# Performance work log

Measured on AMD Instinct MI355X. Metric: run time of the kernel, lower is better.

Reference implementation:

```python
import jax, jax.numpy as jnp
import numpy as np

B_, S, D = 2, 2048, 2048
F_ = 8192
R = 16
H = 16
HD = D // H
MOD_SCALE = 0.1
EPS = 1e-6


def _rmsnorm(x, w):
    v = jnp.mean(x * x, axis=-1, keepdims=True)
    return x * jax.lax.rsqrt(v + EPS) * w


def setup_inputs() -> dict:
    key = jax.random.key(0)
    ks = jax.random.split(key, 12)
    sd = 0.02
    return {
        "hidden_states": jax.random.normal(ks[0], (B_, S, D), jnp.float32),
        "ln1_w": jnp.ones((D,), jnp.float32),
        "ln2_w": jnp.ones((D,), jnp.float32),
        "Wq": jax.random.normal(ks[1], (D, D), jnp.float32) * sd,
        "Wk": jax.random.normal(ks[2], (D, D), jnp.float32) * sd,
        "Wv": jax.random.normal(ks[3], (D, D), jnp.float32) * sd,
        "Wo": jax.random.normal(ks[4], (D, D), jnp.float32) * sd,
        "A": jax.random.normal(ks[5], (D, R), jnp.float32) * (0.01 / np.sqrt(D)),
        "B": jax.random.normal(ks[6], (R, F_), jnp.float32) * (0.01 / np.sqrt(R)),
        "W_in_base": jax.random.normal(ks[7], (F_, D), jnp.float32) * sd,
        "W_up_base": jax.random.normal(ks[8], (F_, D), jnp.float32) * sd,
        "W_down": jax.random.normal(ks[9], (D, F_), jnp.float32) * sd,
    }


def _attention(x, Wq, Wk, Wv, Wo):
    # x: (b, s, d). Causal multi-head self-attention, torch Linear convention (y = x @ W.T).
    b, s, d = x.shape
    q = (x @ Wq.T).reshape(b, s, H, HD)
    k = (x @ Wk.T).reshape(b, s, H, HD)
    v = (x @ Wv.T).reshape(b, s, H, HD)
    scores = jnp.einsum("bqhd,bkhd->bhqk", q, k) / np.sqrt(HD).astype(np.float32)
    causal = jnp.tril(jnp.ones((s, s), bool))
    scores = jnp.where(causal, scores, jnp.finfo(scores.dtype).min)
    probs = jax.nn.softmax(scores, axis=-1)
    out = jnp.einsum("bhqk,bkhd->bqhd", probs, v).reshape(b, s, d)
    return out @ Wo.T


def reference(hidden_states, ln1_w, ln2_w, Wq, Wk, Wv, Wo, A, B, W_in_base, W_up_base, W_down):
    residual = hidden_states
    x = _rmsnorm(hidden_states, ln1_w)
    attn = _attention(x, Wq, Wk, Wv, Wo)  # (b, s, d)

    # NeuroPlasticComponent: delta_w[b,s,d,f] = sum_r mod[b,s,r] * A[d,r] * B[r,f]
    mod = MOD_SCALE * jnp.tanh(attn @ A)  # (b, s, r)

    # NPT quirk: post_attention_layernorm is applied to the ORIGINAL residual,
    # and attention output is never added into the residual stream.
    h = _rmsnorm(residual, ln2_w)  # (b, s, d)

    # Per-token modulated gate: (W_in_base + delta_w[b,s].T) @ h
    # delta_w[b,s].T @ h = sum_d delta[d,f] h[d] = ((mod * (h @ A)) @ B)[f]
    gate_pre = h @ W_in_base.T + (mod * (h @ A)) @ B  # (b, s, f)
    gate = jax.nn.silu(gate_pre)
    up = h @ W_up_base.T
    mlp_out = (gate * up) @ W_down.T
    return residual + mlp_out
```

## Files before the change

kernel.cpp:

```cpp
#include <hip/hip_runtime.h>

#define DI __device__ __forceinline__

typedef short s16x8 __attribute__((ext_vector_type(8)));
typedef float f32x4 __attribute__((ext_vector_type(4)));

typedef __attribute__((address_space(1))) const unsigned int as1_cuint;
typedef __attribute__((address_space(3))) unsigned int as3_uint;

DI unsigned short f2bf(float f) {
  union { float f; unsigned int u; } v; v.f = f;
  unsigned int r = v.u + 0x7fffu + ((v.u >> 16) & 1u);
  return (unsigned short)(r >> 16);
}
DI float bf2f(unsigned short b) {
  union { unsigned int u; float f; } v; v.u = ((unsigned int)b) << 16;
  return v.f;
}

DI void gl_lds16(const void* g, void* l) {
  __builtin_amdgcn_global_load_lds((as1_cuint*)g, (as3_uint*)l, 16, 0, 0);
}

DI void bar() {
  __builtin_amdgcn_sched_barrier(0);
  __builtin_amdgcn_s_barrier();
  __builtin_amdgcn_sched_barrier(0);
}
DI void vm0() { asm volatile("s_waitcnt vmcnt(0)" ::: "memory"); }
DI void vm2() { asm volatile("s_waitcnt vmcnt(2)" ::: "memory"); }
DI void vm4() { asm volatile("s_waitcnt vmcnt(4)" ::: "memory"); }
DI void vm6() { asm volatile("s_waitcnt vmcnt(6)" ::: "memory"); }

#define MFMA __builtin_amdgcn_mfma_f32_16x16x32_bf16

__global__ __launch_bounds__(256) void cvt_f32_bf16(const float* __restrict__ src,
                                                    unsigned short* __restrict__ dst, int n4) {
  int i = blockIdx.x * blockDim.x + threadIdx.x;
  int stride = gridDim.x * blockDim.x;
  for (; i < n4; i += stride) {
    float4 v = ((const float4*)src)[i];
    ((ushort4*)dst)[i] = make_ushort4(f2bf(v.x), f2bf(v.y), f2bf(v.z), f2bf(v.w));
  }
}

__global__ __launch_bounds__(256) void rmsnorm_dual(const float* __restrict__ hs,
                                                    const float* __restrict__ w1,
                                                    const float* __restrict__ w2,
                                                    unsigned short* __restrict__ xo,
                                                    unsigned short* __restrict__ ho) {
  const int D = 2048;
  int t = blockIdx.x, tid = threadIdx.x;
  const float* row = hs + (size_t)t * D;
  float4 a = ((const float4*)row)[tid * 2];
  float4 b = ((const float4*)row)[tid * 2 + 1];
  float ss = a.x * a.x + a.y * a.y + a.z * a.z + a.w * a.w +
             b.x * b.x + b.y * b.y + b.z * b.z + b.w * b.w;
#pragma unroll
  for (int off = 32; off; off >>= 1) ss += __shfl_xor(ss, off);
  __shared__ float red[4];
  int wave = tid >> 6, lane = tid & 63;
  if (lane == 0) red[wave] = ss;
  __syncthreads();
  float tot = red[0] + red[1] + red[2] + red[3];
  float inv = rsqrtf(tot / (float)D + 1e-6f);
  int base = tid * 8;
  float vals[8] = {a.x, a.y, a.z, a.w, b.x, b.y, b.z, b.w};
  float4 w1a = ((const float4*)(w1 + base))[0];
  float4 w1b = ((const float4*)(w1 + base))[1];
  float4 w2a = ((const float4*)(w2 + base))[0];
  float4 w2b = ((const float4*)(w2 + base))[1];
  float w1v[8] = {w1a.x, w1a.y, w1a.z, w1a.w, w1b.x, w1b.y, w1b.z, w1b.w};
  float w2v[8] = {w2a.x, w2a.y, w2a.z, w2a.w, w2b.x, w2b.y, w2b.z, w2b.w};
  unsigned short ox[8], oh[8];
#pragma unroll
  for (int j = 0; j < 8; ++j) {
    float n = vals[j] * inv;
    ox[j] = f2bf(n * w1v[j]);
    oh[j] = f2bf(n * w2v[j]);
  }
  ushort4* xp = (ushort4*)(xo + (size_t)t * D + base);
  ushort4* hp = (ushort4*)(ho + (size_t)t * D + base);
  xp[0] = make_ushort4(ox[0], ox[1], ox[2], ox[3]);
  xp[1] = make_ushort4(ox[4], ox[5], ox[6], ox[7]);
  hp[0] = make_ushort4(oh[0], oh[1], oh[2], oh[3]);
  hp[1] = make_ushort4(oh[4], oh[5], oh[6], oh[7]);
}

#define E_NONE 0
#define E_RES 3

template <int EPI>
__global__ __launch_bounds__(512, 2) void gemm_n128(
    const unsigned short* __restrict__ Amat, const unsigned short* __restrict__ Bt,
    int N, int K, int NT,
    unsigned short* __restrict__ Cbf, float* __restrict__ Cf,
    const float* __restrict__ Res) {
  __shared__ __align__(16) unsigned short lds[49152];
  int tid = threadIdx.x, lane = tid & 63;
  int w = tid >> 6, wm = w >> 2, wn = w & 3;
  int lr = lane & 15, g = lane >> 4;
  int nbn = N >> 7, nwg = gridDim.x, wg = blockIdx.x;
  int cpx = nwg >> 3;
  int swz = (wg & 7) * cpx + (wg >> 3);
  int tm = swz / nbn, tn = swz - tm * nbn;
  size_t m0 = (size_t)tm * 256, n0 = (size_t)tn * 128;

  int boffA[4][2], boffB[2][2];
#pragma unroll
  for (int mi = 0; mi < 4; ++mi)
#pragma unroll
    for (int kh = 0; kh < 2; ++kh) {
      int row = mi * 32 + wm * 16 + lr;
      boffA[mi][kh] = row * 128 + ((kh * 64 + g * 16) ^ ((row & 7) << 4));
    }
#pragma unroll
  for (int ni = 0; ni < 2; ++ni)
#pragma unroll
    for (int kh = 0; kh < 2; ++kh) {
      int row = ni * 64 + wn * 16 + lr;
      boffB[ni][kh] = row * 128 + ((kh * 64 + g * 16) ^ ((row & 7) << 4));
    }
  const char* ldsb = (const char*)lds;

  int srow = tid >> 3;
  int scb = ((tid & 7) * 16) ^ ((srow & 7) << 4);
  const unsigned short* pA0 = Amat + (m0 + srow) * (size_t)K + (scb >> 1);
  const unsigned short* pA1 = pA0 + (size_t)128 * K;
  const unsigned short* pB  = Bt + (n0 + srow) * (size_t)K + (scb >> 1);
  const size_t jst = (size_t)64 * K;
  int dst = w * 512;

  f32x4 acc[8][2] = {};

  auto stg = [&](const unsigned short* p, int BUF, int SLOT) {
    gl_lds16(p, &lds[BUF * 24576 + SLOT * 8192 + dst]);
    gl_lds16(p + jst, &lds[BUF * 24576 + SLOT * 8192 + 4096 + dst]);
  };

  stg(pA0, 0, 0); stg(pB, 0, 2); stg(pA1, 0, 1);
  pA0 += 64; pA1 += 64; pB += 64;
  vm2();
  bar();

  auto tile = [&](int t, int BUF) {
    s16x8 afr[4][2], bfr[2][2];
#pragma unroll
    for (int mi = 0; mi < 4; ++mi)
#pragma unroll
      for (int kh = 0; kh < 2; ++kh)
        afr[mi][kh] = *(const s16x8*)(ldsb + BUF * 49152 + 0 * 16384 + boffA[mi][kh]);
#pragma unroll
    for (int ni = 0; ni < 2; ++ni)
#pragma unroll
      for (int kh = 0; kh < 2; ++kh)
        bfr[ni][kh] = *(const s16x8*)(ldsb + BUF * 49152 + 2 * 16384 + boffB[ni][kh]);
    if (t + 1 < NT) { stg(pA0, BUF ^ 1, 0); stg(pB, BUF ^ 1, 2); }
    bar();
    __builtin_amdgcn_s_setprio(1);
#pragma unroll
    for (int mi = 0; mi < 4; ++mi)
#pragma unroll
      for (int ni = 0; ni < 2; ++ni)
#pragma unroll
        for (int kh = 0; kh < 2; ++kh)
          acc[mi][ni] = MFMA(afr[mi][kh], bfr[ni][kh], acc[mi][ni], 0, 0, 0);
    __builtin_amdgcn_s_setprio(0);
    if (t + 1 < NT) vm4(); else vm0();
    bar();
#pragma unroll
    for (int mi = 0; mi < 4; ++mi)
#pragma unroll
      for (int kh = 0; kh < 2; ++kh)
        afr[mi][kh] = *(const s16x8*)(ldsb + BUF * 49152 + 1 * 16384 + boffA[mi][kh]);
    if (t + 1 < NT) stg(pA1, BUF ^ 1, 1);
    bar();
    __builtin_amdgcn_s_setprio(1);
#pragma unroll
    for (int mi = 0; mi < 4; ++mi)
#pragma unroll
      for (int ni = 0; ni < 2; ++ni)
#pragma unroll
        for (int kh = 0; kh < 2; ++kh)
          acc[4 + mi][ni] = MFMA(afr[mi][kh], bfr[ni][kh], acc[4 + mi][ni], 0, 0, 0);
    __builtin_amdgcn_s_setprio(0);
    if (t + 1 < NT) vm2();
    bar();
    pA0 += 64; pA1 += 64; pB += 64;
  };

  for (int t = 0; t < NT; t += 2) { tile(t, 0); tile(t + 1, 1); }

#pragma unroll
  for (int mh = 0; mh < 2; ++mh)
#pragma unroll
    for (int mi = 0; mi < 4; ++mi)
#pragma unroll
      for (int r = 0; r < 4; ++r) {
        size_t row = m0 + mh * 128 + mi * 32 + wm * 16 + g * 4 + r;
#pragma unroll
        for (int ni = 0; ni < 2; ++ni) {
          size_t col = n0 + ni * 64 + wn * 16 + lr;
          float v = acc[mh * 4 + mi][ni][r];
          if constexpr (EPI == E_RES) Cf[row * N + col] = Res[row * N + col] + v;
          else Cbf[row * N + col] = f2bf(v);
        }
      }
}

__global__ __launch_bounds__(512, 2) void gemm_mlp256(
    const unsigned short* __restrict__ Hm, const unsigned short* __restrict__ Wg,
    const unsigned short* __restrict__ Wu,
    const float* __restrict__ cvec, const float* __restrict__ Bsm,
    unsigned short* __restrict__ Out) {
  const int N = 8192, K = 2048, NT = 32;
  __shared__ __align__(16) unsigned short lds[65536];
  int tid = threadIdx.x, lane = tid & 63;
  int w = tid >> 6, wm = w >> 2, wn = w & 3;
  int lr = lane & 15, g = lane >> 4;
  int nbn = N >> 7, nwg = gridDim.x, wg = blockIdx.x;
  int cpx = nwg >> 3;
  int swz = (wg & 7) * cpx + (wg >> 3);
  int tm = swz / nbn, tn = swz - tm * nbn;
  size_t m0 = (size_t)tm * 256, n0 = (size_t)tn * 128;

  int boffA[4][2], boffB[2][2];
#pragma unroll
  for (int mi = 0; mi < 4; ++mi)
#pragma unroll
    for (int kh = 0; kh < 2; ++kh) {
      int row = mi * 32 + wm * 16 + lr;
      boffA[mi][kh] = row * 128 + ((kh * 64 + g * 16) ^ ((row & 7) << 4));
    }
#pragma unroll
  for (int ni = 0; ni < 2; ++ni)
#pragma unroll
    for (int kh = 0; kh < 2; ++kh) {
      int row = ni * 64 + wn * 16 + lr;
      boffB[ni][kh] = row * 128 + ((kh * 64 + g * 16) ^ ((row & 7) << 4));
    }
  const char* ldsb = (const char*)lds;

  int srow = tid >> 3;
  int scb = ((tid & 7) * 16) ^ ((srow & 7) << 4);
  const unsigned short* pA0 = Hm + (m0 + srow) * (size_t)K + (scb >> 1);
  const unsigned short* pA1 = pA0 + (size_t)128 * K;
  const unsigned short* pBg = Wg + (n0 + srow) * (size_t)K + (scb >> 1);
  const unsigned short* pBu = Wu + (n0 + srow) * (size_t)K + (scb >> 1);
  const size_t jst = (size_t)64 * K;
  int dst = w * 512;

  f32x4 ag[8][2] = {}, au[8][2] = {};

  auto stg = [&](const unsigned short* p, int BUF, int SLOT) {
    gl_lds16(p, &lds[BUF * 32768 + SLOT * 8192 + dst]);
    gl_lds16(p + jst, &lds[BUF * 32768 + SLOT * 8192 + 4096 + dst]);
  };

  stg(pA0, 0, 0); stg(pBg, 0, 2); stg(pBu, 0, 3); stg(pA1, 0, 1);
  pA0 += 64; pA1 += 64; pBg += 64; pBu += 64;
  vm4();
  bar();

  auto tile = [&](int t, int BUF) {
    s16x8 afr[4][2], bg[2][2], bu[2][2];
#pragma unroll
    for (int mi = 0; mi < 4; ++mi)
#pragma unroll
      for (int kh = 0; kh < 2; ++kh)
        afr[mi][kh] = *(const s16x8*)(ldsb + BUF * 65536 + 0 * 16384 + boffA[mi][kh]);
#pragma unroll
    for (int ni = 0; ni < 2; ++ni)
#pragma unroll
      for (int kh = 0; kh < 2; ++kh)
        bg[ni][kh] = *(const s16x8*)(ldsb + BUF * 65536 + 2 * 16384 + boffB[ni][kh]);
    if (t + 1 < NT) { stg(pA0, BUF ^ 1, 0); stg(pBg, BUF ^ 1, 2); }
    bar();
    __builtin_amdgcn_s_setprio(1);
#pragma unroll
    for (int mi = 0; mi < 4; ++mi)
#pragma unroll
      for (int ni = 0; ni < 2; ++ni)
#pragma unroll
        for (int kh = 0; kh < 2; ++kh)
          ag[mi][ni] = MFMA(afr[mi][kh], bg[ni][kh], ag[mi][ni], 0, 0, 0);
    __builtin_amdgcn_s_setprio(0);
    if (t + 1 < NT) vm6(); else vm2();
    bar();
#pragma unroll
    for (int ni = 0; ni < 2; ++ni)
#pragma unroll
      for (int kh = 0; kh < 2; ++kh)
        bu[ni][kh] = *(const s16x8*)(ldsb + BUF * 65536 + 3 * 16384 + boffB[ni][kh]);
    if (t + 1 < NT) stg(pBu, BUF ^ 1, 3);
    bar();
    __builtin_amdgcn_s_setprio(1);
#pragma unroll
    for (int mi = 0; mi < 4; ++mi)
#pragma unroll
      for (int ni = 0; ni < 2; ++ni)
#pragma unroll
        for (int kh = 0; kh < 2; ++kh)
          au[mi][ni] = MFMA(afr[mi][kh], bu[ni][kh], au[mi][ni], 0, 0, 0);
    __builtin_amdgcn_s_setprio(0);
    if (t + 1 < NT) vm6(); else vm0();
    bar();
#pragma unroll
    for (int mi = 0; mi < 4; ++mi)
#pragma unroll
      for (int kh = 0; kh < 2; ++kh)
        afr[mi][kh] = *(const s16x8*)(ldsb + BUF * 65536 + 1 * 16384 + boffA[mi][kh]);
    if (t + 1 < NT) stg(pA1, BUF ^ 1, 1);
    bar();
    __builtin_amdgcn_s_setprio(1);
#pragma unroll
    for (int mi = 0; mi < 4; ++mi)
#pragma unroll
      for (int ni = 0; ni < 2; ++ni)
#pragma unroll
        for (int kh = 0; kh < 2; ++kh)
          ag[4 + mi][ni] = MFMA(afr[mi][kh], bg[ni][kh], ag[4 + mi][ni], 0, 0, 0);
    __builtin_amdgcn_s_setprio(0);
    bar();
    __builtin_amdgcn_s_setprio(1);
#pragma unroll
    for (int mi = 0; mi < 4; ++mi)
#pragma unroll
      for (int ni = 0; ni < 2; ++ni)
#pragma unroll
        for (int kh = 0; kh < 2; ++kh)
          au[4 + mi][ni] = MFMA(afr[mi][kh], bu[ni][kh], au[4 + mi][ni], 0, 0, 0);
    __builtin_amdgcn_s_setprio(0);
    if (t + 1 < NT) vm4();
    bar();
    pA0 += 64; pA1 += 64; pBg += 64; pBu += 64;
  };

  for (int t = 0; t < NT; t += 2) { tile(t, 0); tile(t + 1, 1); }

  float* cl = (float*)lds;
  float* bl = (float*)&lds[32768];
#pragma unroll
  for (int j = 0; j < 2; ++j) {
    int fi = tid * 2 + j;
    ((float4*)cl)[fi] = ((const float4*)(cvec + m0 * 16))[fi];
  }
  {
    int fi = tid;
    ((float4*)bl)[fi] = *(const float4*)(Bsm + (size_t)(fi >> 5) * N + n0 + (fi & 31) * 4);
  }
  bar();

#pragma unroll
  for (int mh = 0; mh < 2; ++mh)
#pragma unroll
    for (int mi = 0; mi < 4; ++mi)
#pragma unroll
      for (int r = 0; r < 4; ++r) {
        int rr = mh * 128 + mi * 32 + wm * 16 + g * 4 + r;
        size_t row = m0 + rr;
#pragma unroll
        for (int ni = 0; ni < 2; ++ni) {
          int cc = ni * 64 + wn * 16 + lr;
          size_t col = n0 + cc;
          float s = 0.f;
#pragma unroll
          for (int jj = 0; jj < 16; ++jj) s += cl[rr * 16 + jj] * bl[jj * 128 + cc];
          float gg = ag[mh * 4 + mi][ni][r] + s;
          float sig = 1.f / (1.f + __expf(-gg));
          Out[row * N + col] = f2bf(gg * sig * au[mh * 4 + mi][ni][r]);
        }
      }
}

__global__ __launch_bounds__(256) void vtrans(const unsigned short* __restrict__ qkv,
                                              unsigned short* __restrict__ vT) {
  __shared__ unsigned short t[64][72];
  int bh = blockIdx.z, b = bh >> 4, h = bh & 15;
  int k0 = blockIdx.x * 64, d0 = blockIdx.y * 64;
  int tid = threadIdx.x;
#pragma unroll
  for (int j = 0; j < 2; ++j) {
    int idx = tid + j * 256;
    int r = idx >> 3, c8 = (idx & 7) * 8;
    s16x8 v = *(const s16x8*)(qkv + ((size_t)(b * 2048 + k0 + r)) * 6144 + 4096 + h * 128 + d0 + c8);
#pragma unroll
    for (int e = 0; e < 8; ++e) t[r][c8 + e] = (unsigned short)v[e];
  }
  __syncthreads();
#pragma unroll
  for (int j = 0; j < 2; ++j) {
    int idx = tid + j * 256;
    int dr = idx >> 3, k8 = (idx & 7) * 8;
    s16x8 o;
#pragma unroll
    for (int e = 0; e < 8; ++e) o[e] = (short)t[k8 + e][dr];
    *(s16x8*)(vT + (size_t)bh * 262144 + (size_t)(d0 + dr) * 2048 + k0 + k8) = o;
  }
}

__global__ __launch_bounds__(256, 2) void attn_fwd2(const unsigned short* __restrict__ qkv,
                                                    const unsigned short* __restrict__ vT,
                                                    unsigned short* __restrict__ attn) {
  const int LD = 6144;
  __shared__ __align__(16) unsigned short Kt[8192];
  __shared__ __align__(16) unsigned short Vt[8192];
  __shared__ __align__(16) unsigned short Pl[4096];
  int tid = threadIdx.x, w = tid >> 6, lane = tid & 63;
  int lrow = lane & 15, g = lane >> 4;
  int qp = blockIdx.x, bh = blockIdx.y, b = bh >> 4, h = bh & 15;
  const unsigned short* Qb = qkv + (size_t)b * 2048 * LD + h * 128;
  const unsigned short* Kb = Qb + 2048;
  const unsigned short* vTb = vT + (size_t)bh * 262144;
  const float scale = 0.08838834764831845f;

#pragma unroll
  for (int pass = 0; pass < 2; ++pass) {
    int qtile = pass ? (31 - qp) : qp;
    int wq0 = qtile * 64 + w * 16;
    s16x8 qf[4];
#pragma unroll
    for (int kc = 0; kc < 4; ++kc)
      qf[kc] = *(const s16x8*)(Qb + (size_t)(wq0 + lrow) * LD + kc * 32 + g * 8);
    f32x4 ao[8] = {};
    float m_r[4], l_r[4];
#pragma unroll
    for (int r = 0; r < 4; ++r) { m_r[r] = -1e30f; l_r[r] = 0.f; }
    int nkt = qtile + 1;

    for (int kt = 0; kt < nkt; ++kt) {
      int k0 = kt * 64;
      bar();
#pragma unroll
      for (int j = 0; j < 4; ++j) {
        int o = j * 4096 + tid * 16;
        int row = o >> 8, cb = o & 255;
        int scb = cb ^ ((row & 7) << 4);
        gl_lds16(Kb + (size_t)(k0 + row) * LD + (scb >> 1), &Kt[(j * 4096 + w * 1024) >> 1]);
      }
#pragma unroll
      for (int j = 0; j < 4; ++j) {
        int o = j * 4096 + tid * 16;
        int row = o >> 7, cb = o & 127;
        int scb = cb ^ ((row & 7) << 4);
        gl_lds16(vTb + (size_t)row * 2048 + k0 + (scb >> 1), &Vt[(j * 4096 + w * 1024) >> 1]);
      }
      vm0();
      bar();
      f32x4 sa[4] = {};
#pragma unroll
      for (int ni = 0; ni < 4; ++ni)
#pragma unroll
        for (int kc = 0; kc < 4; ++kc) {
          int row = ni * 16 + lrow;
          int cb = kc * 64 + g * 16;
          int scb = cb ^ ((row & 7) << 4);
          s16x8 kf = *(const s16x8*)&Kt[row * 128 + (scb >> 1)];
          sa[ni] = MFMA(qf[kc], kf, sa[ni], 0, 0, 0);
        }
      if (k0 + 63 > wq0) {
#pragma unroll
        for (int ni = 0; ni < 4; ++ni)
#pragma unroll
          for (int r = 0; r < 4; ++r) {
            int q_idx = wq0 + g * 4 + r, k_idx = k0 + ni * 16 + lrow;
            float sv = sa[ni][r] * scale;
            sa[ni][r] = (k_idx > q_idx) ? -1e30f : sv;
          }
      } else {
#pragma unroll
        for (int ni = 0; ni < 4; ++ni)
#pragma unroll
          for (int r = 0; r < 4; ++r) sa[ni][r] *= scale;
      }
      float mt[4];
#pragma unroll
      for (int r = 0; r < 4; ++r)
        mt[r] = fmaxf(fmaxf(sa[0][r], sa[1][r]), fmaxf(sa[2][r], sa[3][r]));
#pragma unroll
      for (int r = 0; r < 4; ++r)
#pragma unroll
        for (int off = 8; off; off >>= 1) mt[r] = fmaxf(mt[r], __shfl_xor(mt[r], off));
      float al[4];
#pragma unroll
      for (int r = 0; r < 4; ++r) {
        float mn = fmaxf(m_r[r], mt[r]);
        al[r] = __expf(m_r[r] - mn);
        m_r[r] = mn;
      }
      float rs[4] = {0.f, 0.f, 0.f, 0.f};
#pragma unroll
      for (int ni = 0; ni < 4; ++ni)
#pragma unroll
        for (int r = 0; r < 4; ++r) {
          float p = __expf(sa[ni][r] - m_r[r]);
          rs[r] += p;
          int q = g * 4 + r, k = ni * 16 + lrow;
          Pl[w * 1024 + q * 64 + (k ^ ((q & 7) << 3))] = f2bf(p);
        }
#pragma unroll
      for (int r = 0; r < 4; ++r) {
#pragma unroll
        for (int off = 8; off; off >>= 1) rs[r] += __shfl_xor(rs[r], off);
        l_r[r] = l_r[r] * al[r] + rs[r];
      }
#pragma unroll
      for (int df = 0; df < 8; ++df)
#pragma unroll
        for (int r = 0; r < 4; ++r) ao[df][r] *= al[r];
      asm volatile("s_waitcnt lgkmcnt(0)" ::: "memory");
      __builtin_amdgcn_sched_barrier(0);
      s16x8 pa[2];
#pragma unroll
      for (int ks = 0; ks < 2; ++ks)
        pa[ks] = *(const s16x8*)&Pl[w * 1024 + lrow * 64 + ((ks * 32 + g * 8) ^ ((lrow & 7) << 3))];
#pragma unroll
      for (int df = 0; df < 8; ++df) {
#pragma unroll
        for (int ks = 0; ks < 2; ++ks) {
          int row = df * 16 + lrow;
          int cb = ks * 64 + g * 16;
          int scb = cb ^ ((row & 7) << 4);
          s16x8 vf = *(const s16x8*)&Vt[row * 64 + (scb >> 1)];
          ao[df] = MFMA(pa[ks], vf, ao[df], 0, 0, 0);
        }
      }
    }
#pragma unroll
    for (int df = 0; df < 8; ++df)
#pragma unroll
      for (int r = 0; r < 4; ++r) {
        int q = wq0 + g * 4 + r;
        float v = ao[df][r] / l_r[r];
        attn[((size_t)b * 2048 + q) * 2048 + h * 128 + df * 16 + lrow] = f2bf(v);
      }
    bar();
  }
}

__global__ __launch_bounds__(256) void modc(const unsigned short* __restrict__ attnO,
                                            const unsigned short* __restrict__ h,
                                            const float* __restrict__ A,
                                            float* __restrict__ cvec) {
  const int D = 2048;
  int t = blockIdx.x * 4 + (threadIdx.x >> 6);
  int lane = threadIdx.x & 63;
  float aA[16] = {}, aH[16] = {};
  for (int i = 0; i < D / 64; ++i) {
    int d = i * 64 + lane;
    float av = bf2f(attnO[(size_t)t * D + d]);
    float hv = bf2f(h[(size_t)t * D + d]);
    const float* ar = A + (size_t)d * 16;
#pragma unroll
    for (int j = 0; j < 16; ++j) {
      float a = ar[j];
      aA[j] += av * a;
      aH[j] += hv * a;
    }
  }
#pragma unroll
  for (int j = 0; j < 16; ++j) {
#pragma unroll
    for (int off = 32; off; off >>= 1) {
      aA[j] += __shfl_xor(aA[j], off);
      aH[j] += __shfl_xor(aH[j], off);
    }
  }
#pragma unroll
  for (int j = 0; j < 16; ++j)
    if (lane == j) cvec[(size_t)t * 16 + j] = 0.1f * tanhf(aA[j]) * aH[j];
}

extern "C" void kernel_launch(void* const* d_in, const int* in_sizes, int n_in,
                              void* d_out, int out_size, void* d_ws, size_t ws_size,
                              hipStream_t stream) {
  const float* hs  = (const float*)d_in[0];
  const float* ln1 = (const float*)d_in[1];
  const float* ln2 = (const float*)d_in[2];
  const float* Wq  = (const float*)d_in[3];
  const float* Wk  = (const float*)d_in[4];
  const float* Wv  = (const float*)d_in[5];
  const float* Wo  = (const float*)d_in[6];
  const float* Am  = (const float*)d_in[7];
  const float* Bm  = (const float*)d_in[8];
  const float* Win = (const float*)d_in[9];
  const float* Wup = (const float*)d_in[10];
  const float* Wdn = (const float*)d_in[11];
  float* out = (float*)d_out;
  (void)in_sizes; (void)n_in;

  const int T = 4096;
  const int Dm = 2048, F = 8192;
  const size_t MB = (size_t)1 << 20;

  const size_t need = 184 * MB;
  if (ws_size < need) {
    hipMemsetAsync(d_out, 0, (size_t)out_size * 4, stream);
    return;
  }
  char* base = (char*)d_ws;
  unsigned short* tb    = (unsigned short*)(base);
  unsigned short* wqkv  = (unsigned short*)(base);
  unsigned short* vT    = (unsigned short*)(base);
  unsigned short* xb    = (unsigned short*)(base + 24 * MB);
  unsigned short* attnO = (unsigned short*)(base + 40 * MB);
  unsigned short* qkv   = (unsigned short*)(base + 64 * MB);
  unsigned short* win   = (unsigned short*)(base + 64 * MB);
  unsigned short* wo    = (unsigned short*)(base + 112 * MB);
  unsigned short* hb    = (unsigned short*)(base + 120 * MB);
  unsigned short* attn  = (unsigned short*)(base + 136 * MB);
  float*          cv    = (float*)(base + 136 * MB);
  unsigned short* wup   = (unsigned short*)(base + 152 * MB);
  unsigned short* wdn   = (unsigned short*)(base + 152 * MB);

  cvt_f32_bf16<<<2048, 256, 0, stream>>>(Wq, wqkv, Dm * Dm / 4);
  cvt_f32_bf16<<<2048, 256, 0, stream>>>(Wk, wqkv + (size_t)Dm * Dm, Dm * Dm / 4);
  cvt_f32_bf16<<<2048, 256, 0, stream>>>(Wv, wqkv + (size_t)2 * Dm * Dm, Dm * Dm / 4);
  cvt_f32_bf16<<<2048, 256, 0, stream>>>(Wo, wo, Dm * Dm / 4);
  rmsnorm_dual<<<T, 256, 0, stream>>>(hs, ln1, ln2, xb, hb);

  gemm_n128<E_NONE><<<(T / 256) * (3 * Dm / 128), 512, 0, stream>>>(
      xb, wqkv, 3 * Dm, Dm, Dm / 64, qkv, nullptr, nullptr);

  vtrans<<<dim3(32, 2, 32), 256, 0, stream>>>(qkv, vT);
  attn_fwd2<<<dim3(16, 32), 256, 0, stream>>>(qkv, vT, attn);

  gemm_n128<E_NONE><<<(T / 256) * (Dm / 128), 512, 0, stream>>>(
      attn, wo, Dm, Dm, Dm / 64, attnO, nullptr, nullptr);

  modc<<<T / 4, 256, 0, stream>>>(attnO, hb, Am, cv);

  cvt_f32_bf16<<<2048, 256, 0, stream>>>(Win, win, F * Dm / 4);
  cvt_f32_bf16<<<2048, 256, 0, stream>>>(Wup, wup, F * Dm / 4);

  gemm_mlp256<<<(T / 256) * (F / 128), 512, 0, stream>>>(hb, win, wup, cv, Bm, tb);

  cvt_f32_bf16<<<2048, 256, 0, stream>>>(Wdn, wdn, Dm * F / 4);
  gemm_n128<E_RES><<<(T / 256) * (Dm / 128), 512, 0, stream>>>(
      tb, wdn, Dm, F, F / 64, nullptr, out, hs);
}
```

Before: 792.0 us.

## Issue all next-tile prefetches at once and merge gate/up MFMA phases

```diff
diff --git a/kernel.cpp b/kernel.cpp
--- a/kernel.cpp
+++ b/kernel.cpp
@@ -29,8 +29,8 @@
 }
 DI void vm0() { asm volatile("s_waitcnt vmcnt(0)" ::: "memory"); }
 DI void vm2() { asm volatile("s_waitcnt vmcnt(2)" ::: "memory"); }
-DI void vm4() { asm volatile("s_waitcnt vmcnt(4)" ::: "memory"); }
 DI void vm6() { asm volatile("s_waitcnt vmcnt(6)" ::: "memory"); }
+DI void vm8() { asm volatile("s_waitcnt vmcnt(8)" ::: "memory"); }
 
 #define MFMA __builtin_amdgcn_mfma_f32_16x16x32_bf16
 
@@ -137,13 +137,18 @@
     gl_lds16(p, &lds[BUF * 24576 + SLOT * 8192 + dst]);
     gl_lds16(p + jst, &lds[BUF * 24576 + SLOT * 8192 + 4096 + dst]);
   };
-
-  stg(pA0, 0, 0); stg(pB, 0, 2); stg(pA1, 0, 1);
-  pA0 += 64; pA1 += 64; pB += 64;
+  auto stg_all = [&](int BUF) {
+    stg(pA0, BUF, 0); stg(pB, BUF, 2); stg(pA1, BUF, 1);
+    pA0 += 64; pB += 64; pA1 += 64;
+  };
+
+  stg_all(0);
   vm2();
   bar();
 
-  auto tile = [&](int t, int BUF) {
+  for (int t = 0; t < NT; ++t) {
+    int BUF = t & 1;
+    bool lastt = (t == NT - 1);
     s16x8 afr[4][2], bfr[2][2];
 #pragma unroll
     for (int mi = 0; mi < 4; ++mi)
@@ -155,7 +160,7 @@
 #pragma unroll
       for (int kh = 0; kh < 2; ++kh)
         bfr[ni][kh] = *(const s16x8*)(ldsb + BUF * 49152 + 2 * 16384 + boffB[ni][kh]);
-    if (t + 1 < NT) { stg(pA0, BUF ^ 1, 0); stg(pB, BUF ^ 1, 2); }
+    if (!lastt) stg_all(BUF ^ 1);
     bar();
     __builtin_amdgcn_s_setprio(1);
 #pragma unroll
@@ -166,14 +171,13 @@
         for (int kh = 0; kh < 2; ++kh)
           acc[mi][ni] = MFMA(afr[mi][kh], bfr[ni][kh], acc[mi][ni], 0, 0, 0);
     __builtin_amdgcn_s_setprio(0);
-    if (t + 1 < NT) vm4(); else vm0();
+    if (lastt) vm0(); else vm6();
     bar();
 #pragma unroll
     for (int mi = 0; mi < 4; ++mi)
 #pragma unroll
       for (int kh = 0; kh < 2; ++kh)
         afr[mi][kh] = *(const s16x8*)(ldsb + BUF * 49152 + 1 * 16384 + boffA[mi][kh]);
-    if (t + 1 < NT) stg(pA1, BUF ^ 1, 1);
     bar();
     __builtin_amdgcn_s_setprio(1);
 #pragma unroll
@@ -184,12 +188,9 @@
         for (int kh = 0; kh < 2; ++kh)
           acc[4 + mi][ni] = MFMA(afr[mi][kh], bfr[ni][kh], acc[4 + mi][ni], 0, 0, 0);
     __builtin_amdgcn_s_setprio(0);
-    if (t + 1 < NT) vm2();
-    bar();
-    pA0 += 64; pA1 += 64; pB += 64;
-  };
-
-  for (int t = 0; t < NT; t += 2) { tile(t, 0); tile(t + 1, 1); }
+    if (!lastt) vm2();
+    bar();
+  }
 
 #pragma unroll
   for (int mh = 0; mh < 2; ++mh)
@@ -256,13 +257,18 @@
     gl_lds16(p, &lds[BUF * 32768 + SLOT * 8192 + dst]);
     gl_lds16(p + jst, &lds[BUF * 32768 + SLOT * 8192 + 4096 + dst]);
   };
-
-  stg(pA0, 0, 0); stg(pBg, 0, 2); stg(pBu, 0, 3); stg(pA1, 0, 1);
-  pA0 += 64; pA1 += 64; pBg += 64; pBu += 64;
-  vm4();
+  auto stg_all = [&](int BUF) {
+    stg(pA0, BUF, 0); stg(pBg, BUF, 2); stg(pBu, BUF, 3); stg(pA1, BUF, 1);
+    pA0 += 64; pBg += 64; pBu += 64; pA1 += 64;
+  };
+
+  stg_all(0);
+  vm2();
   bar();
 
-  auto tile = [&](int t, int BUF) {
+  for (int t = 0; t < NT; ++t) {
+    int BUF = t & 1;
+    bool lastt = (t == NT - 1);
     s16x8 afr[4][2], bg[2][2], bu[2][2];
 #pragma unroll
     for (int mi = 0; mi < 4; ++mi)
@@ -272,9 +278,11 @@
 #pragma unroll
     for (int ni = 0; ni < 2; ++ni)
 #pragma unroll
-      for (int kh = 0; kh < 2; ++kh)
+      for (int kh = 0; kh < 2; ++kh) {
         bg[ni][kh] = *(const s16x8*)(ldsb + BUF * 65536 + 2 * 16384 + boffB[ni][kh]);
-    if (t + 1 < NT) { stg(pA0, BUF ^ 1, 0); stg(pBg, BUF ^ 1, 2); }
+        bu[ni][kh] = *(const s16x8*)(ldsb + BUF * 65536 + 3 * 16384 + boffB[ni][kh]);
+      }
+    if (!lastt) stg_all(BUF ^ 1);
     bar();
     __builtin_amdgcn_s_setprio(1);
 #pragma unroll
@@ -282,35 +290,18 @@
 #pragma unroll
       for (int ni = 0; ni < 2; ++ni)
 #pragma unroll
-        for (int kh = 0; kh < 2; ++kh)
+        for (int kh = 0; kh < 2; ++kh) {
           ag[mi][ni] = MFMA(afr[mi][kh], bg[ni][kh], ag[mi][ni], 0, 0, 0);
+          au[mi][ni] = MFMA(afr[mi][kh], bu[ni][kh], au[mi][ni], 0, 0, 0);
+        }
     __builtin_amdgcn_s_setprio(0);
-    if (t + 1 < NT) vm6(); else vm2();
-    bar();
-#pragma unroll
-    for (int ni = 0; ni < 2; ++ni)
-#pragma unroll
-      for (int kh = 0; kh < 2; ++kh)
-        bu[ni][kh] = *(const s16x8*)(ldsb + BUF * 65536 + 3 * 16384 + boffB[ni][kh]);
-    if (t + 1 < NT) stg(pBu, BUF ^ 1, 3);
-    bar();
-    __builtin_amdgcn_s_setprio(1);
-#pragma unroll
-    for (int mi = 0; mi < 4; ++mi)
-#pragma unroll
-      for (int ni = 0; ni < 2; ++ni)
-#pragma unroll
-        for (int kh = 0; kh < 2; ++kh)
-          au[mi][ni] = MFMA(afr[mi][kh], bu[ni][kh], au[mi][ni], 0, 0, 0);
-    __builtin_amdgcn_s_setprio(0);
-    if (t + 1 < NT) vm6(); else vm0();
+    if (lastt) vm0(); else vm8();
     bar();
 #pragma unroll
     for (int mi = 0; mi < 4; ++mi)
 #pragma unroll
       for (int kh = 0; kh < 2; ++kh)
         afr[mi][kh] = *(const s16x8*)(ldsb + BUF * 65536 + 1 * 16384 + boffA[mi][kh]);
-    if (t + 1 < NT) stg(pA1, BUF ^ 1, 1);
     bar();
     __builtin_amdgcn_s_setprio(1);
 #pragma unroll
@@ -318,25 +309,14 @@
 #pragma unroll
       for (int ni = 0; ni < 2; ++ni)
 #pragma unroll
-        for (int kh = 0; kh < 2; ++kh)
+        for (int kh = 0; kh < 2; ++kh) {
           ag[4 + mi][ni] = MFMA(afr[mi][kh], bg[ni][kh], ag[4 + mi][ni], 0, 0, 0);
+          au[4 + mi][ni] = MFMA(afr[mi][kh], bu[ni][kh], au[4 + mi][ni], 0, 0, 0);
+        }
     __builtin_amdgcn_s_setprio(0);
-    bar();
-    __builtin_amdgcn_s_setprio(1);
-#pragma unroll
-    for (int mi = 0; mi < 4; ++mi)
-#pragma unroll
-      for (int ni = 0; ni < 2; ++ni)
-#pragma unroll
-        for (int kh = 0; kh < 2; ++kh)
-          au[4 + mi][ni] = MFMA(afr[mi][kh], bu[ni][kh], au[4 + mi][ni], 0, 0, 0);
-    __builtin_amdgcn_s_setprio(0);
-    if (t + 1 < NT) vm4();
-    bar();
-    pA0 += 64; pA1 += 64; pBg += 64; pBu += 64;
-  };
-
-  for (int t = 0; t < NT; t += 2) { tile(t, 0); tile(t + 1, 1); }
+    if (!lastt) vm2();
+    bar();
+  }
 
   float* cl = (float*)lds;
   float* bl = (float*)&lds[32768];
```

New measurement: 810.7 us. 2.3% more time.

## Simplify generic GEMM to single-buffer sync loop; restructure MLP GEMM prefetch schedule

Applied to the files above, without the earlier changes.

```diff
diff --git a/kernel.cpp b/kernel.cpp
--- a/kernel.cpp
+++ b/kernel.cpp
@@ -28,11 +28,28 @@
   __builtin_amdgcn_sched_barrier(0);
 }
 DI void vm0() { asm volatile("s_waitcnt vmcnt(0)" ::: "memory"); }
-DI void vm2() { asm volatile("s_waitcnt vmcnt(2)" ::: "memory"); }
-DI void vm4() { asm volatile("s_waitcnt vmcnt(4)" ::: "memory"); }
 DI void vm6() { asm volatile("s_waitcnt vmcnt(6)" ::: "memory"); }
+DI void sfence() { __builtin_amdgcn_sched_barrier(0); }
 
 #define MFMA __builtin_amdgcn_mfma_f32_16x16x32_bf16
+
+DI void stage_half(const unsigned short* gb, size_t r0, int K, int kt,
+                   unsigned short* lh, int tid) {
+#pragma unroll
+  for (int j = 0; j < 2; ++j) {
+    int o = j * 8192 + tid * 16;
+    int row = o >> 7, cb = o & 127;
+    int scb = cb ^ ((row & 7) << 4);
+    gl_lds16(gb + (r0 + row) * (size_t)K + kt + (scb >> 1),
+             lh + ((j * 8192 + (tid >> 6) * 1024) >> 1));
+  }
+}
+
+DI s16x8 rd_frag(const unsigned short* lds, int baseE, int rwh, int kh, int lane) {
+  int cb = kh * 64 + ((lane >> 4) << 4);
+  int scb = cb ^ ((rwh & 7) << 4);
+  return *(const s16x8*)&lds[baseE + rwh * 64 + (scb >> 1)];
+}
 
 __global__ __launch_bounds__(256) void cvt_f32_bf16(const float* __restrict__ src,
                                                     unsigned short* __restrict__ dst, int n4) {
@@ -133,30 +150,31 @@
 
   f32x4 acc[8][2] = {};
 
-  auto stg = [&](const unsigned short* p, int BUF, int SLOT) {
-    gl_lds16(p, &lds[BUF * 24576 + SLOT * 8192 + dst]);
-    gl_lds16(p + jst, &lds[BUF * 24576 + SLOT * 8192 + 4096 + dst]);
+  auto stg = [&](const unsigned short* p, int SLOT) {
+    gl_lds16(p, &lds[SLOT * 8192 + dst]);
+    gl_lds16(p + jst, &lds[SLOT * 8192 + 4096 + dst]);
   };
-
-  stg(pA0, 0, 0); stg(pB, 0, 2); stg(pA1, 0, 1);
-  pA0 += 64; pA1 += 64; pB += 64;
-  vm2();
-  bar();
-
-  auto tile = [&](int t, int BUF) {
+  auto stg_all = [&]() {
+    stg(pA0, 0); stg(pA1, 1); stg(pB, 2);
+    pA0 += 64; pA1 += 64; pB += 64;
+  };
+
+  for (int t = 0; t < NT; ++t) {
+    bar();
+    stg_all();
+    vm0();
+    bar();
     s16x8 afr[4][2], bfr[2][2];
 #pragma unroll
     for (int mi = 0; mi < 4; ++mi)
 #pragma unroll
       for (int kh = 0; kh < 2; ++kh)
-        afr[mi][kh] = *(const s16x8*)(ldsb + BUF * 49152 + 0 * 16384 + boffA[mi][kh]);
+        afr[mi][kh] = *(const s16x8*)(ldsb + 0 * 16384 + boffA[mi][kh]);
 #pragma unroll
     for (int ni = 0; ni < 2; ++ni)
 #pragma unroll
       for (int kh = 0; kh < 2; ++kh)
-        bfr[ni][kh] = *(const s16x8*)(ldsb + BUF * 49152 + 2 * 16384 + boffB[ni][kh]);
-    if (t + 1 < NT) { stg(pA0, BUF ^ 1, 0); stg(pB, BUF ^ 1, 2); }
-    bar();
+        bfr[ni][kh] = *(const s16x8*)(ldsb + 2 * 16384 + boffB[ni][kh]);
     __builtin_amdgcn_s_setprio(1);
 #pragma unroll
     for (int mi = 0; mi < 4; ++mi)
@@ -166,15 +184,12 @@
         for (int kh = 0; kh < 2; ++kh)
           acc[mi][ni] = MFMA(afr[mi][kh], bfr[ni][kh], acc[mi][ni], 0, 0, 0);
     __builtin_amdgcn_s_setprio(0);
-    if (t + 1 < NT) vm4(); else vm0();
-    bar();
+    s16x8 af1[4][2];
 #pragma unroll
     for (int mi = 0; mi < 4; ++mi)
 #pragma unroll
       for (int kh = 0; kh < 2; ++kh)
-        afr[mi][kh] = *(const s16x8*)(ldsb + BUF * 49152 + 1 * 16384 + boffA[mi][kh]);
-    if (t + 1 < NT) stg(pA1, BUF ^ 1, 1);
-    bar();
+        af1[mi][kh] = *(const s16x8*)(ldsb + 1 * 16384 + boffA[mi][kh]);
     __builtin_amdgcn_s_setprio(1);
 #pragma unroll
     for (int mi = 0; mi < 4; ++mi)
@@ -182,14 +197,9 @@
       for (int ni = 0; ni < 2; ++ni)
 #pragma unroll
         for (int kh = 0; kh < 2; ++kh)
-          acc[4 + mi][ni] = MFMA(afr[mi][kh], bfr[ni][kh], acc[4 + mi][ni], 0, 0, 0);
+          acc[4 + mi][ni] = MFMA(af1[mi][kh], bfr[ni][kh], acc[4 + mi][ni], 0, 0, 0);
     __builtin_amdgcn_s_setprio(0);
-    if (t + 1 < NT) vm2();
-    bar();
-    pA0 += 64; pA1 += 64; pB += 64;
-  };
-
-  for (int t = 0; t < NT; t += 2) { tile(t, 0); tile(t + 1, 1); }
+  }
 
 #pragma unroll
   for (int mh = 0; mh < 2; ++mh)
@@ -217,64 +227,42 @@
   __shared__ __align__(16) unsigned short lds[65536];
   int tid = threadIdx.x, lane = tid & 63;
   int w = tid >> 6, wm = w >> 2, wn = w & 3;
-  int lr = lane & 15, g = lane >> 4;
-  int nbn = N >> 7, nwg = gridDim.x, wg = blockIdx.x;
+  int lr = lane & 15, lkh = lane >> 4;
+  int nbn = 64;
+  int nwg = gridDim.x, wg = blockIdx.x;
   int cpx = nwg >> 3;
   int swz = (wg & 7) * cpx + (wg >> 3);
   int tm = swz / nbn, tn = swz - tm * nbn;
   size_t m0 = (size_t)tm * 256, n0 = (size_t)tn * 128;
 
-  int boffA[4][2], boffB[2][2];
-#pragma unroll
-  for (int mi = 0; mi < 4; ++mi)
-#pragma unroll
-    for (int kh = 0; kh < 2; ++kh) {
-      int row = mi * 32 + wm * 16 + lr;
-      boffA[mi][kh] = row * 128 + ((kh * 64 + g * 16) ^ ((row & 7) << 4));
-    }
-#pragma unroll
-  for (int ni = 0; ni < 2; ++ni)
-#pragma unroll
-    for (int kh = 0; kh < 2; ++kh) {
-      int row = ni * 64 + wn * 16 + lr;
-      boffB[ni][kh] = row * 128 + ((kh * 64 + g * 16) ^ ((row & 7) << 4));
-    }
-  const char* ldsb = (const char*)lds;
-
-  int srow = tid >> 3;
-  int scb = ((tid & 7) * 16) ^ ((srow & 7) << 4);
-  const unsigned short* pA0 = Hm + (m0 + srow) * (size_t)K + (scb >> 1);
-  const unsigned short* pA1 = pA0 + (size_t)128 * K;
-  const unsigned short* pBg = Wg + (n0 + srow) * (size_t)K + (scb >> 1);
-  const unsigned short* pBu = Wu + (n0 + srow) * (size_t)K + (scb >> 1);
-  const size_t jst = (size_t)64 * K;
-  int dst = w * 512;
-
-  f32x4 ag[8][2] = {}, au[8][2] = {};
-
-  auto stg = [&](const unsigned short* p, int BUF, int SLOT) {
-    gl_lds16(p, &lds[BUF * 32768 + SLOT * 8192 + dst]);
-    gl_lds16(p + jst, &lds[BUF * 32768 + SLOT * 8192 + 4096 + dst]);
+  auto stage = [&](int tau, int slot) {
+    if (tau >= NT) return;
+    const unsigned short* gb = (slot == 2) ? Wg : (slot == 3) ? Wu : Hm;
+    size_t r0 = (slot >= 2) ? n0 : (m0 + (size_t)slot * 128);
+    stage_half(gb, r0, K, tau * 64, &lds[(tau & 1) * 32768 + slot * 8192], tid);
   };
 
-  stg(pA0, 0, 0); stg(pBg, 0, 2); stg(pBu, 0, 3); stg(pA1, 0, 1);
-  pA0 += 64; pA1 += 64; pBg += 64; pBu += 64;
-  vm4();
+  stage(0, 0); stage(0, 2); stage(0, 1); stage(0, 3);
+  stage(1, 0); stage(1, 2); stage(1, 1);
+  vm6();
   bar();
 
-  auto tile = [&](int t, int BUF) {
-    s16x8 afr[4][2], bg[2][2], bu[2][2];
+  f32x4 acc[8][4] = {};
+  s16x8 afr[4][2], bfr[2][2][2];
+
+  for (int t = 0; t < NT; ++t) {
+    int buf = (t & 1) * 32768;
 #pragma unroll
     for (int mi = 0; mi < 4; ++mi)
 #pragma unroll
       for (int kh = 0; kh < 2; ++kh)
-        afr[mi][kh] = *(const s16x8*)(ldsb + BUF * 65536 + 0 * 16384 + boffA[mi][kh]);
+        afr[mi][kh] = rd_frag(lds, buf + 0 * 8192, mi * 32 + wm * 16 + lr, kh, lane);
 #pragma unroll
     for (int ni = 0; ni < 2; ++ni)
 #pragma unroll
       for (int kh = 0; kh < 2; ++kh)
-        bg[ni][kh] = *(const s16x8*)(ldsb + BUF * 65536 + 2 * 16384 + boffB[ni][kh]);
-    if (t + 1 < NT) { stg(pA0, BUF ^ 1, 0); stg(pBg, BUF ^ 1, 2); }
+        bfr[0][ni][kh] = rd_frag(lds, buf + 2 * 8192, ni * 64 + wn * 16 + lr, kh, lane);
+    stage(t + 1, 3);
     bar();
     __builtin_amdgcn_s_setprio(1);
 #pragma unroll
@@ -283,16 +271,15 @@
       for (int ni = 0; ni < 2; ++ni)
 #pragma unroll
         for (int kh = 0; kh < 2; ++kh)
-          ag[mi][ni] = MFMA(afr[mi][kh], bg[ni][kh], ag[mi][ni], 0, 0, 0);
+          acc[mi][ni] = MFMA(afr[mi][kh], bfr[0][ni][kh], acc[mi][ni], 0, 0, 0);
     __builtin_amdgcn_s_setprio(0);
-    if (t + 1 < NT) vm6(); else vm2();
     bar();
 #pragma unroll
     for (int ni = 0; ni < 2; ++ni)
 #pragma unroll
       for (int kh = 0; kh < 2; ++kh)
-        bu[ni][kh] = *(const s16x8*)(ldsb + BUF * 65536 + 3 * 16384 + boffB[ni][kh]);
-    if (t + 1 < NT) stg(pBu, BUF ^ 1, 3);
+        bfr[1][ni][kh] = rd_frag(lds, buf + 3 * 8192, ni * 64 + wn * 16 + lr, kh, lane);
+    stage(t + 2, 0);
     bar();
     __builtin_amdgcn_s_setprio(1);
 #pragma unroll
@@ -301,16 +288,15 @@
       for (int ni = 0; ni < 2; ++ni)
 #pragma unroll
         for (int kh = 0; kh < 2; ++kh)
-          au[mi][ni] = MFMA(afr[mi][kh], bu[ni][kh], au[mi][ni], 0, 0, 0);
+          acc[mi][2 + ni] = MFMA(afr[mi][kh], bfr[1][ni][kh], acc[mi][2 + ni], 0, 0, 0);
     __builtin_amdgcn_s_setprio(0);
-    if (t + 1 < NT) vm6(); else vm0();
     bar();
 #pragma unroll
     for (int mi = 0; mi < 4; ++mi)
 #pragma unroll
       for (int kh = 0; kh < 2; ++kh)
-        afr[mi][kh] = *(const s16x8*)(ldsb + BUF * 65536 + 1 * 16384 + boffA[mi][kh]);
-    if (t + 1 < NT) stg(pA1, BUF ^ 1, 1);
+        afr[mi][kh] = rd_frag(lds, buf + 1 * 8192, mi * 32 + wm * 16 + lr, kh, lane);
+    stage(t + 2, 2);
     bar();
     __builtin_amdgcn_s_setprio(1);
 #pragma unroll
@@ -319,9 +305,11 @@
       for (int ni = 0; ni < 2; ++ni)
 #pragma unroll
         for (int kh = 0; kh < 2; ++kh)
-          ag[4 + mi][ni] = MFMA(afr[mi][kh], bg[ni][kh], ag[4 + mi][ni], 0, 0, 0);
+          acc[4 + mi][ni] = MFMA(afr[mi][kh], bfr[0][ni][kh], acc[4 + mi][ni], 0, 0, 0);
     __builtin_amdgcn_s_setprio(0);
     bar();
+    stage(t + 2, 1);
+    bar();
     __builtin_amdgcn_s_setprio(1);
 #pragma unroll
     for (int mi = 0; mi < 4; ++mi)
@@ -329,17 +317,15 @@
       for (int ni = 0; ni < 2; ++ni)
 #pragma unroll
         for (int kh = 0; kh < 2; ++kh)
-          au[4 + mi][ni] = MFMA(afr[mi][kh], bu[ni][kh], au[4 + mi][ni], 0, 0, 0);
+          acc[4 + mi][2 + ni] = MFMA(afr[mi][kh], bfr[1][ni][kh], acc[4 + mi][2 + ni], 0, 0, 0);
     __builtin_amdgcn_s_setprio(0);
-    if (t + 1 < NT) vm4();
-    bar();
-    pA0 += 64; pA1 += 64; pBg += 64; pBu += 64;
-  };
-
-  for (int t = 0; t < NT; t += 2) { tile(t, 0); tile(t + 1, 1); }
+    if (t < NT - 2) vm6();
+    else if (t == NT - 2) vm0();
+    bar();
+  }
 
   float* cl = (float*)lds;
-  float* bl = (float*)&lds[32768];
+  float* bl = (float*)&lds[16384];
 #pragma unroll
   for (int j = 0; j < 2; ++j) {
     int fi = tid * 2 + j;
@@ -357,18 +343,19 @@
     for (int mi = 0; mi < 4; ++mi)
 #pragma unroll
       for (int r = 0; r < 4; ++r) {
-        int rr = mh * 128 + mi * 32 + wm * 16 + g * 4 + r;
+        int rr = mh * 128 + mi * 32 + wm * 16 + lkh * 4 + r;
         size_t row = m0 + rr;
 #pragma unroll
         for (int ni = 0; ni < 2; ++ni) {
-          int cc = ni * 64 + wn * 16 + lr;
-          size_t col = n0 + cc;
+          int coff = ni * 64 + wn * 16 + lr;
+          size_t col = n0 + coff;
           float s = 0.f;
 #pragma unroll
-          for (int jj = 0; jj < 16; ++jj) s += cl[rr * 16 + jj] * bl[jj * 128 + cc];
-          float gg = ag[mh * 4 + mi][ni][r] + s;
+          for (int jj = 0; jj < 16; ++jj) s += cl[rr * 16 + jj] * bl[jj * 128 + coff];
+          float gg = acc[mh * 4 + mi][ni][r] + s;
+          float uu = acc[mh * 4 + mi][2 + ni][r];
           float sig = 1.f / (1.f + __expf(-gg));
-          Out[row * N + col] = f2bf(gg * sig * au[mh * 4 + mi][ni][r]);
+          Out[row * N + col] = f2bf(gg * sig * uu);
         }
       }
 }
```

New measurement: 894.8 us. 1.13x slower.
